# Optimization experiments

Measured on AMD Instinct MI355X. Metric: run time of the kernel, lower is better.

Reference implementation:

```python
import jax, jax.numpy as jnp
import numpy as np

E_LAYERS = (0, 1, 2, 3, 4, 5)
E_P_LENGTH = 8  # prompt_param[1]
COS_EPS = 1e-6


def setup_inputs() -> dict:
    key = jax.random.key(0)
    k1, k2, k3, k4, k5 = jax.random.split(key, 5)
    B, C = 1024, 768
    POOL, D = 100, 768
    return {
        "x_querry": jax.random.normal(k1, (B, C), dtype=jnp.float32),
        "x_block": jax.random.normal(k2, (B, 197, D), dtype=jnp.float32),
        "K": jax.random.uniform(k3, (POOL, C), dtype=jnp.float32),
        "A": jax.random.uniform(k4, (POOL, C), dtype=jnp.float32),
        "p": jax.random.uniform(k5, (E_P_LENGTH, POOL, D), dtype=jnp.float32),
        "l": 0,
    }


def reference(x_querry, x_block, K, A, p, l):
    # Eval-mode forward (train=False, expand_and_freeze=False, full pool used).
    if l not in E_LAYERS:
        return (None, 0, x_block)
    # a_querry = einsum('bd,kd->bkd', x_querry, softmax(A, dim=1))
    A_sm = jax.nn.softmax(A, axis=1)                       # [K, d]
    a_querry = x_querry[:, None, :] * A_sm[None, :, :]     # [B, K, d]
    # CosineSimilarity(dim=2, eps=1e-6): dot / (max(||a||, eps) * max(||K||, eps))
    dots = jnp.einsum('bkd,kd->bk', a_querry, K)           # [B, K]
    a_norm = jnp.maximum(jnp.sqrt(jnp.sum(a_querry * a_querry, axis=2)), COS_EPS)
    k_norm = jnp.maximum(jnp.sqrt(jnp.sum(K * K, axis=1)), COS_EPS)
    aq_k = dots / (a_norm * k_norm[None, :])
    aq_k = (aq_k + 1.0) / 2.0                              # [B, K] in [0, 1]
    # weighted prompt combination: P_ = einsum('bk,lkd->bld', aq_k, p)
    P_ = jnp.einsum('bk,lkd->bld', aq_k, p)                # [B, L, d]
    i = E_P_LENGTH // 2
    Ek = P_[:, :i, :]
    Ev = P_[:, i:, :]
    return (Ek, Ev, x_block)
```

## Files before the change

### kernel.cpp

```cpp
#include <hip/hip_runtime.h>
#include <math.h>

#define B_SZ   1024
#define CDIM   768
#define POOL   100
#define COSEPS 1e-6f
#define NTHR   256
#define BATCH4 2048

typedef __attribute__((ext_vector_type(4))) float f32x4;

#define LOAD8(v, base)                                                       \
    do { const f32x4* _s = (base);                                           \
         v##0 = _s[0];        v##1 = _s[NTHR];     v##2 = _s[2 * NTHR];      \
         v##3 = _s[3 * NTHR]; v##4 = _s[4 * NTHR]; v##5 = _s[5 * NTHR];      \
         v##6 = _s[6 * NTHR]; v##7 = _s[7 * NTHR]; } while (0)
#define STORE8(v, base)                                                      \
    do { f32x4* _d = (base);                                                 \
         _d[0] = v##0;        _d[NTHR] = v##1;     _d[2 * NTHR] = v##2;      \
         _d[3 * NTHR] = v##3; _d[4 * NTHR] = v##4; _d[5 * NTHR] = v##5;      \
         _d[6 * NTHR] = v##6; _d[7 * NTHR] = v##7; } while (0)

__device__ __forceinline__ void copy_pipe(const f32x4* __restrict__ src,
                                          f32x4* __restrict__ dst,
                                          int b0, int b1, int cid, int nblk, int t) {
    int btA = b0 + cid;
    if (btA >= b1) return;
    f32x4 va0, va1, va2, va3, va4, va5, va6, va7;
    f32x4 vb0, vb1, vb2, vb3, vb4, vb5, vb6, vb7;
    LOAD8(va, src + (size_t)btA * BATCH4 + t);
    int btB = btA + nblk;
    while (btB < b1) {
        LOAD8(vb, src + (size_t)btB * BATCH4 + t);
        STORE8(va, dst + (size_t)btA * BATCH4 + t);
        btA = btB; btB += nblk;
        if (btB >= b1) {
            STORE8(vb, dst + (size_t)btA * BATCH4 + t);
            return;
        }
        LOAD8(va, src + (size_t)btB * BATCH4 + t);
        STORE8(vb, dst + (size_t)btA * BATCH4 + t);
        btA = btB; btB += nblk;
    }
    STORE8(va, dst + (size_t)btA * BATCH4 + t);
}

__global__ __launch_bounds__(NTHR)
void k1_prep_copy(const float* __restrict__ A, const float* __restrict__ K,
                  float* __restrict__ W1, float* __restrict__ W2,
                  float* __restrict__ knorm,
                  const f32x4* __restrict__ src4, f32x4* __restrict__ dst4,
                  int nb1) {
    const int blk = blockIdx.x, t = threadIdx.x;
    if (blk < POOL) {
        __shared__ float red[NTHR];
        const int k = blk;
        const float* Ar = A + (size_t)k * CDIM;
        const float* Kr = K + (size_t)k * CDIM;

        float m = -INFINITY;
        for (int d = t; d < CDIM; d += NTHR) m = fmaxf(m, Ar[d]);
        red[t] = m; __syncthreads();
        for (int s = 128; s > 0; s >>= 1) { if (t < s) red[t] = fmaxf(red[t], red[t + s]); __syncthreads(); }
        m = red[0]; __syncthreads();

        float sum = 0.f;
        for (int d = t; d < CDIM; d += NTHR) sum += expf(Ar[d] - m);
        red[t] = sum; __syncthreads();
        for (int s = 128; s > 0; s >>= 1) { if (t < s) red[t] += red[t + s]; __syncthreads(); }
        sum = red[0]; __syncthreads();
        const float inv = 1.0f / sum;

        float ksq = 0.f;
        for (int d = t; d < CDIM; d += NTHR) { float kv = Kr[d]; ksq += kv * kv; }
        red[t] = ksq; __syncthreads();
        for (int s = 128; s > 0; s >>= 1) { if (t < s) red[t] += red[t + s]; __syncthreads(); }
        if (t == 0) knorm[k] = fmaxf(sqrtf(red[0]), COSEPS);

        for (int d = t; d < CDIM; d += NTHR) {
            float a_sm = expf(Ar[d] - m) * inv;
            W1[(size_t)k * CDIM + d] = a_sm * Kr[d];
            W2[(size_t)k * CDIM + d] = a_sm * a_sm;
        }
        __syncthreads();
    }
    copy_pipe(src4, dst4, 0, nb1, blk, (int)gridDim.x, t);
}

__global__ __launch_bounds__(NTHR)
void k2_aq_copy(const float* __restrict__ xq,
                const float* __restrict__ W1, const float* __restrict__ W2,
                const float* __restrict__ knorm, float* __restrict__ aq,
                const f32x4* __restrict__ src4, f32x4* __restrict__ dst4,
                int nb1, int nb2) {
    const int blk = blockIdx.x, t = threadIdx.x;
    const int role = (blk >> 3) & 1;
    const int id   = ((blk >> 4) << 3) | (blk & 7);

    if (role) {
        copy_pipe(src4, dst4, nb1, nb2, id, 1024, t);
        return;
    }

    __shared__ f32x4 xs4[CDIM / 4];
    const int b = id;
    const f32x4* xq4 = (const f32x4*)(xq + (size_t)b * CDIM);
    for (int i = t; i < CDIM / 4; i += NTHR) xs4[i] = xq4[i];
    __syncthreads();

    const int wave = t >> 6, lane = t & 63;
    for (int k = wave; k < POOL; k += 4) {
        const f32x4* w14 = (const f32x4*)(W1 + (size_t)k * CDIM);
        const f32x4* w24 = (const f32x4*)(W2 + (size_t)k * CDIM);
        float s1 = 0.f, s2 = 0.f;
        #pragma unroll
        for (int i = 0; i < CDIM / 4 / 64; ++i) {
            const int d4 = lane + i * 64;
            f32x4 x  = xs4[d4];
            f32x4 w1 = w14[d4];
            f32x4 w2 = w24[d4];
            s1 += x.x * w1.x + x.y * w1.y + x.z * w1.z + x.w * w1.w;
            s2 += x.x * x.x * w2.x + x.y * x.y * w2.y
                + x.z * x.z * w2.z + x.w * x.w * w2.w;
        }
        for (int off = 32; off > 0; off >>= 1) {
            s1 += __shfl_down(s1, off);
            s2 += __shfl_down(s2, off);
        }
        if (lane == 0) {
            float an = fmaxf(sqrtf(s2), COSEPS);
            float v  = s1 / (an * knorm[k]);
            aq[(size_t)b * POOL + k] = (v + 1.0f) * 0.5f;
        }
    }
}

__global__ __launch_bounds__(NTHR)
void k3_p_copy(const float* __restrict__ aq, const float* __restrict__ p,
               float* __restrict__ out,
               const f32x4* __restrict__ src4, f32x4* __restrict__ dst4,
               int nb2, int NB, int n4) {
    const int blk = blockIdx.x, t = threadIdx.x;
    const int role = (blk >> 3) & 1;
    const int id   = ((blk >> 4) << 3) | (blk & 7);

    if (role) {
        copy_pipe(src4, dst4, nb2, NB, id, 1024, t);
        for (int i = NB * BATCH4 + id * NTHR + t; i < n4; i += 1024 * NTHR)
            dst4[i] = src4[i];
        return;
    }

    __shared__ float a_s[POOL * 8];
    const int l  = id & 7;
    const int bg = id >> 3;

    for (int i = t; i < POOL * 8; i += NTHR) {
        int bb = i & 7, k = i >> 3;
        a_s[i] = aq[(size_t)(bg * 8 + bb) * POOL + k];
    }
    __syncthreads();

    const float* pl = p + (size_t)l * POOL * CDIM + t;
    float acc[8][3];
    #pragma unroll
    for (int bb = 0; bb < 8; ++bb)
        #pragma unroll
        for (int j = 0; j < 3; ++j) acc[bb][j] = 0.f;

    for (int k = 0; k < POOL; ++k) {
        float p0 = pl[(size_t)k * CDIM];
        float p1 = pl[(size_t)k * CDIM + 256];
        float p2 = pl[(size_t)k * CDIM + 512];
        #pragma unroll
        for (int bb = 0; bb < 8; ++bb) {
            float a = a_s[k * 8 + bb];
            acc[bb][0] += a * p0;
            acc[bb][1] += a * p1;
            acc[bb][2] += a * p2;
        }
    }

    const size_t EK_SZ = (size_t)B_SZ * 4 * CDIM;
    #pragma unroll
    for (int bb = 0; bb < 8; ++bb) {
        int b = bg * 8 + bb;
        float* dst = (l < 4)
            ? out + (size_t)b * (4 * CDIM) + (size_t)l * CDIM
            : out + EK_SZ + (size_t)b * (4 * CDIM) + (size_t)(l - 4) * CDIM;
        dst[t]       = acc[bb][0];
        dst[t + 256] = acc[bb][1];
        dst[t + 512] = acc[bb][2];
    }
}

extern "C" void kernel_launch(void* const* d_in, const int* in_sizes, int n_in,
                              void* d_out, int out_size, void* d_ws, size_t ws_size,
                              hipStream_t stream) {
    const float* x_querry = (const float*)d_in[0];
    const float* x_block  = (const float*)d_in[1];
    const float* K        = (const float*)d_in[2];
    const float* A        = (const float*)d_in[3];
    const float* p        = (const float*)d_in[4];
    float* out = (float*)d_out;

    float* W1    = (float*)d_ws;
    float* W2    = W1 + POOL * CDIM;
    float* knorm = W2 + POOL * CDIM;
    float* aq    = knorm + 128;

    const size_t EK_SZ = (size_t)B_SZ * 4 * CDIM;
    const f32x4* src4 = (const f32x4*)x_block;
    f32x4* dst4 = (f32x4*)(out + 2 * EK_SZ);

    const int n4 = in_sizes[1] / 4;
    const int NB = n4 / BATCH4;

    const int u16 = NB / 16;
    const int nb1 = u16 * 8;
    const int nb2 = u16 * 12;

    k1_prep_copy<<<1024, NTHR, 0, stream>>>(A, K, W1, W2, knorm, src4, dst4, nb1);
    k2_aq_copy  <<<2048, NTHR, 0, stream>>>(x_querry, W1, W2, knorm, aq,
                                            src4, dst4, nb1, nb2);
    k3_p_copy   <<<2048, NTHR, 0, stream>>>(aq, p, out, src4, dst4,
                                            nb2, NB, n4);
}
```

Baseline: 257.9 us.

## Move x_block copy out of prep kernel and split it evenly across later kernels

The prep kernel now runs only the 100 softmax/norm blocks instead of also carrying part of the x_block passthrough copy. The copy is divided in half between the aq kernel and the prompt-combination kernel, so each copies half instead of 4/8 and 4/8 of the remaining quarter-splits. This shortens the first kernel and rebalances the copy work onto kernels that have compute to overlap with. The risk is that the first kernel's small grid leaves the GPU idle and the later kernels' copy halves become the critical path.

```diff
diff --git a/kernel.cpp b/kernel.cpp
--- a/kernel.cpp
+++ b/kernel.cpp
@@ -46,45 +46,39 @@
 }
 
 __global__ __launch_bounds__(NTHR)
-void k1_prep_copy(const float* __restrict__ A, const float* __restrict__ K,
-                  float* __restrict__ W1, float* __restrict__ W2,
-                  float* __restrict__ knorm,
-                  const f32x4* __restrict__ src4, f32x4* __restrict__ dst4,
-                  int nb1) {
+void k1_prep(const float* __restrict__ A, const float* __restrict__ K,
+             float* __restrict__ W1, float* __restrict__ W2,
+             float* __restrict__ knorm) {
     const int blk = blockIdx.x, t = threadIdx.x;
-    if (blk < POOL) {
-        __shared__ float red[NTHR];
-        const int k = blk;
-        const float* Ar = A + (size_t)k * CDIM;
-        const float* Kr = K + (size_t)k * CDIM;
-
-        float m = -INFINITY;
-        for (int d = t; d < CDIM; d += NTHR) m = fmaxf(m, Ar[d]);
-        red[t] = m; __syncthreads();
-        for (int s = 128; s > 0; s >>= 1) { if (t < s) red[t] = fmaxf(red[t], red[t + s]); __syncthreads(); }
-        m = red[0]; __syncthreads();
-
-        float sum = 0.f;
-        for (int d = t; d < CDIM; d += NTHR) sum += expf(Ar[d] - m);
-        red[t] = sum; __syncthreads();
-        for (int s = 128; s > 0; s >>= 1) { if (t < s) red[t] += red[t + s]; __syncthreads(); }
-        sum = red[0]; __syncthreads();
-        const float inv = 1.0f / sum;
-
-        float ksq = 0.f;
-        for (int d = t; d < CDIM; d += NTHR) { float kv = Kr[d]; ksq += kv * kv; }
-        red[t] = ksq; __syncthreads();
-        for (int s = 128; s > 0; s >>= 1) { if (t < s) red[t] += red[t + s]; __syncthreads(); }
-        if (t == 0) knorm[k] = fmaxf(sqrtf(red[0]), COSEPS);
-
-        for (int d = t; d < CDIM; d += NTHR) {
-            float a_sm = expf(Ar[d] - m) * inv;
-            W1[(size_t)k * CDIM + d] = a_sm * Kr[d];
-            W2[(size_t)k * CDIM + d] = a_sm * a_sm;
-        }
-        __syncthreads();
-    }
-    copy_pipe(src4, dst4, 0, nb1, blk, (int)gridDim.x, t);
+    __shared__ float red[NTHR];
+    const int k = blk;
+    const float* Ar = A + (size_t)k * CDIM;
+    const float* Kr = K + (size_t)k * CDIM;
+
+    float m = -INFINITY;
+    for (int d = t; d < CDIM; d += NTHR) m = fmaxf(m, Ar[d]);
+    red[t] = m; __syncthreads();
+    for (int s = 128; s > 0; s >>= 1) { if (t < s) red[t] = fmaxf(red[t], red[t + s]); __syncthreads(); }
+    m = red[0]; __syncthreads();
+
+    float sum = 0.f;
+    for (int d = t; d < CDIM; d += NTHR) sum += expf(Ar[d] - m);
+    red[t] = sum; __syncthreads();
+    for (int s = 128; s > 0; s >>= 1) { if (t < s) red[t] += red[t + s]; __syncthreads(); }
+    sum = red[0]; __syncthreads();
+    const float inv = 1.0f / sum;
+
+    float ksq = 0.f;
+    for (int d = t; d < CDIM; d += NTHR) { float kv = Kr[d]; ksq += kv * kv; }
+    red[t] = ksq; __syncthreads();
+    for (int s = 128; s > 0; s >>= 1) { if (t < s) red[t] += red[t + s]; __syncthreads(); }
+    if (t == 0) knorm[k] = fmaxf(sqrtf(red[0]), COSEPS);
+
+    for (int d = t; d < CDIM; d += NTHR) {
+        float a_sm = expf(Ar[d] - m) * inv;
+        W1[(size_t)k * CDIM + d] = a_sm * Kr[d];
+        W2[(size_t)k * CDIM + d] = a_sm * a_sm;
+    }
 }
 
 __global__ __launch_bounds__(NTHR)
@@ -92,13 +86,13 @@
                 const float* __restrict__ W1, const float* __restrict__ W2,
                 const float* __restrict__ knorm, float* __restrict__ aq,
                 const f32x4* __restrict__ src4, f32x4* __restrict__ dst4,
-                int nb1, int nb2) {
+                int nbH) {
     const int blk = blockIdx.x, t = threadIdx.x;
     const int role = (blk >> 3) & 1;
     const int id   = ((blk >> 4) << 3) | (blk & 7);
 
     if (role) {
-        copy_pipe(src4, dst4, nb1, nb2, id, 1024, t);
+        copy_pipe(src4, dst4, 0, nbH, id, 1024, t);
         return;
     }
 
@@ -139,13 +133,13 @@
 void k3_p_copy(const float* __restrict__ aq, const float* __restrict__ p,
                float* __restrict__ out,
                const f32x4* __restrict__ src4, f32x4* __restrict__ dst4,
-               int nb2, int NB, int n4) {
+               int nbH, int NB, int n4) {
     const int blk = blockIdx.x, t = threadIdx.x;
     const int role = (blk >> 3) & 1;
     const int id   = ((blk >> 4) << 3) | (blk & 7);
 
     if (role) {
-        copy_pipe(src4, dst4, nb2, NB, id, 1024, t);
+        copy_pipe(src4, dst4, nbH, NB, id, 1024, t);
         for (int i = NB * BATCH4 + id * NTHR + t; i < n4; i += 1024 * NTHR)
             dst4[i] = src4[i];
         return;
@@ -215,14 +209,11 @@
 
     const int n4 = in_sizes[1] / 4;
     const int NB = n4 / BATCH4;
-
-    const int u16 = NB / 16;
-    const int nb1 = u16 * 8;
-    const int nb2 = u16 * 12;
-
-    k1_prep_copy<<<1024, NTHR, 0, stream>>>(A, K, W1, W2, knorm, src4, dst4, nb1);
-    k2_aq_copy  <<<2048, NTHR, 0, stream>>>(x_querry, W1, W2, knorm, aq,
-                                            src4, dst4, nb1, nb2);
-    k3_p_copy   <<<2048, NTHR, 0, stream>>>(aq, p, out, src4, dst4,
-                                            nb2, NB, n4);
-}
+    const int nbH = NB / 2;
+
+    k1_prep   <<<POOL, NTHR, 0, stream>>>(A, K, W1, W2, knorm);
+    k2_aq_copy<<<2048, NTHR, 0, stream>>>(x_querry, W1, W2, knorm, aq,
+                                          src4, dst4, nbH);
+    k3_p_copy <<<2048, NTHR, 0, stream>>>(aq, p, out, src4, dst4,
+                                          nbH, NB, n4);
+}
```

Result: slower. 270.1 us (+4.7%).
